# Performance work log

Hardware: AMD Instinct MI355X
Metric: run time of the kernel (lower is better)

The kernel has to match this reference:

```python
import jax, jax.numpy as jnp
import numpy as np

B, T, C, H = 2, 2048, 1024, 16
D = C // H  # head dim = 64

def setup_inputs() -> dict:
    key = jax.random.key(0)
    k1, k2 = jax.random.split(key)
    x = jax.random.normal(k1, (B, T, C), dtype=jnp.float32)
    W_attn = jax.random.normal(k2, (3 * C, C), dtype=jnp.float32) * 0.02
    return {"x": x, "W_attn": W_attn}

def reference(x, W_attn):
    Bx, Tx, Cx = x.shape
    qkv = jnp.einsum('btc,fc->btf', x, W_attn)  # fused QKV projection (bias=False)
    q, k, v = jnp.split(qkv, 3, axis=-1)
    # [B, H, T, D]
    q = q.reshape(Bx, Tx, H, D).transpose(0, 2, 1, 3)
    k = k.reshape(Bx, Tx, H, D).transpose(0, 2, 1, 3)
    v = v.reshape(Bx, Tx, H, D).transpose(0, 2, 1, 3)
    scale = 1.0 / jnp.sqrt(jnp.asarray(D, dtype=q.dtype))
    scores = jnp.einsum('bhqd,bhkd->bhqk', q, k) * scale  # [B,H,T,T]
    causal = jnp.tril(jnp.ones((Tx, Tx), dtype=bool))
    scores = jnp.where(causal[None, None], scores, jnp.asarray(-jnp.inf, dtype=scores.dtype))
    attn = jax.nn.softmax(scores, axis=-1)
    y = jnp.einsum('bhqk,bhkd->bhqd', attn, v)
    y = y.transpose(0, 2, 1, 3).reshape(Bx, Tx, Cx)  # merge heads; dropout=0 at eval
    return y
```

## Files before the change

### kernel.cpp

```cpp
#include <hip/hip_runtime.h>
#include <hip/hip_bf16.h>

#define Bn 2
#define Tn 2048
#define Cn 1024
#define Hn 16
#define Dn 64
#define Mdim 4096
#define Ndim 3072
#define Kdim 1024

typedef unsigned short u16;
typedef __attribute__((ext_vector_type(8))) short bf16x8;
typedef __attribute__((ext_vector_type(4))) float f32x4;

__device__ __forceinline__ u16 f2bf(float v) {
    unsigned int x = __builtin_bit_cast(unsigned int, v);
    unsigned int r = (x + 0x7fffu + ((x >> 16) & 1u)) >> 16;
    return (u16)r;
}

__device__ __forceinline__ unsigned int cvt_pk_bf16(float lo, float hi) {
    unsigned int r;
    asm("v_cvt_pk_bf16_f32 %0, %1, %2" : "=v"(r) : "v"(lo), "v"(hi));
    return r;
}

__device__ __forceinline__ void async16(const void* g, void* l) {
    __builtin_amdgcn_global_load_lds(
        (const __attribute__((address_space(1))) void*)g,
        (__attribute__((address_space(3))) void*)(unsigned int)(unsigned long long)l,
        16, 0, 0);
}

__device__ __forceinline__ int probe_inline(const unsigned int* __restrict__ X, int tid) {
    const int lane = tid & 63;
    int cnt = 0;
    #pragma unroll
    for (int i = 0; i < 8; i++) {
        unsigned int e = (X[lane * 8 + i] >> 7) & 0xFFu;
        cnt += (e >= 100u && e < 134u) ? 1 : 0;
    }
    #pragma unroll
    for (int off = 1; off < 64; off <<= 1) cnt += __shfl_xor(cnt, off);
    return cnt > 256 ? 1 : 0;
}

#define NXC ((size_t)Mdim * Kdim / 8)
#define NWC ((size_t)Ndim * Kdim / 8)

__global__ __launch_bounds__(256) void convert_in(
        const void* __restrict__ Xv, const void* __restrict__ Wv,
        u16* __restrict__ Xb, u16* __restrict__ Wb, int* __restrict__ flag) {
    const int isbf = probe_inline((const unsigned int*)Xv, threadIdx.x);
    if (blockIdx.x == 0 && threadIdx.x == 0) *flag = isbf;
    size_t i = (size_t)blockIdx.x * 256 + threadIdx.x;
    if (i >= NXC + NWC) return;
    const void* src; u16* dst; size_t off;
    if (i < NXC) { src = Xv; dst = Xb; off = i; }
    else         { src = Wv; dst = Wb; off = i - NXC; }
    if (isbf) {
        ((uint4*)dst)[off] = ((const uint4*)src)[off];
    } else {
        const float4* s = (const float4*)src + off * 2;
        float4 a = s[0], b = s[1];
        ((uint4*)dst)[off] = (uint4){cvt_pk_bf16(a.x, a.y), cvt_pk_bf16(a.z, a.w),
                                     cvt_pk_bf16(b.x, b.y), cvt_pk_bf16(b.z, b.w)};
    }
}

#define NTq (Kdim / 64)
#define QSCL 0.1803368867f

#define PBAR() do { asm volatile("" ::: "memory"); \
                    __builtin_amdgcn_s_barrier();  \
                    asm volatile("" ::: "memory"); } while (0)
#define VMW(n) asm volatile("s_waitcnt vmcnt(" #n ")" ::: "memory")

#define STGA(QIDX, BUF, KOFF) \
    async16(Xb + (size_t)(m0 + (QIDX) * 64 + srow) * Kdim + (KOFF) + gc, \
            &sA[BUF][(QIDX) * 4096 + w * 512])
#define STGB(QIDX, BUF, KOFF) \
    async16(Wb + (size_t)(n0 + (QIDX) * 64 + srow) * Kdim + (KOFF) + gc, \
            &sB[BUF][(QIDX) * 4096 + w * 512])

#define RDAh(FR, MQ, BUF) do {                                             \
    _Pragma("unroll")                                                      \
    for (int mt = 0; mt < 4; mt++) {                                       \
        const u16* p = &sA[BUF][(wm + (MQ) * 64 + mt * 16 + r16) * 64];    \
        FR[mt][0] = *(const bf16x8*)(p + cx0);                             \
        FR[mt][1] = *(const bf16x8*)(p + (cx0 ^ 32));                      \
    } } while (0)

#define RDBall(BUF) do {                                                   \
    _Pragma("unroll")                                                      \
    for (int nt = 0; nt < 3; nt++) {                                       \
        const u16* p = &sB[BUF][(wn + nt * 16 + r16) * 64];                \
        bfr[nt][0] = *(const bf16x8*)(p + cx0);                            \
        bfr[nt][1] = *(const bf16x8*)(p + (cx0 ^ 32));                     \
    } } while (0)

#define MMH(BASE, FR) do {                                                 \
    _Pragma("unroll")                                                      \
    for (int mt = 0; mt < 4; mt++)                                         \
        _Pragma("unroll")                                                  \
        for (int nt = 0; nt < 3; nt++) {                                   \
            acc[(BASE)+mt][nt] = __builtin_amdgcn_mfma_f32_16x16x32_bf16(  \
                FR[mt][0], bfr[nt][0], acc[(BASE)+mt][nt], 0, 0, 0);       \
            acc[(BASE)+mt][nt] = __builtin_amdgcn_mfma_f32_16x16x32_bf16(  \
                FR[mt][1], bfr[nt][1], acc[(BASE)+mt][nt], 0, 0, 0);       \
        }                                                                  \
} while (0)

__global__ __launch_bounds__(512, 2) void qkv_gemm(
        const u16* __restrict__ Xb, const u16* __restrict__ Wb,
        u16* __restrict__ Q, u16* __restrict__ Kc, u16* __restrict__ Vt) {
    __shared__ __align__(16) u16 sA[2][256 * 64];
    __shared__ __align__(16) u16 sB[2][192 * 64];

    const int tid  = threadIdx.x;
    const int lane = tid & 63;
    const int w    = tid >> 6;
    const int quad = lane >> 4;
    const int r16  = lane & 15;
    const int wm   = (w >> 2) * 128;
    const int wn   = (w & 3) * 48;

    const int l0 = blockIdx.x;
    const int nl = (l0 & 7) * 32 + (l0 >> 3);
    const int m0 = (nl >> 4) * 256;
    const int n0 = (nl & 15) * 192;

    const int lr   = lane >> 3;
    const int gc   = ((lane & 7) ^ lr) * 8;
    const int srow = w * 8 + lr;

    const int cx0 = (quad ^ (r16 & 7)) * 8;

    f32x4 acc[8][3];
    #pragma unroll
    for (int i = 0; i < 8; i++)
        #pragma unroll
        for (int j = 0; j < 3; j++)
            acc[i][j] = (f32x4){0.f, 0.f, 0.f, 0.f};

    bf16x8 af[4][2], ag[4][2];
    bf16x8 bfr[3][2];

    #pragma unroll
    for (int q = 0; q < 4; q++) STGA(q, 0, 0);
    #pragma unroll
    for (int q = 0; q < 3; q++) STGB(q, 0, 0);
    STGA(0, 1, 64); STGA(2, 1, 64); STGB(0, 1, 64); STGB(1, 1, 64);
    VMW(4);
    PBAR();

    int koff = 0;
    for (int kt = 0; kt < NTq; kt++) {
        const int cur = kt & 1, nxt = cur ^ 1;
        const int kn = koff + 64, kn2 = koff + 128;
        if (kt + 1 < NTq) { STGA(1, nxt, kn); STGA(3, nxt, kn); STGB(2, nxt, kn); }
        RDAh(af, 0, cur);
        RDBall(cur);
        PBAR();
        __builtin_amdgcn_s_setprio(1);
        MMH(0, af);
        __builtin_amdgcn_s_setprio(0);
        PBAR();
        RDAh(ag, 1, cur);
        if (kt + 2 < NTq) { STGA(0, cur, kn2); STGA(2, cur, kn2);
                            STGB(0, cur, kn2); STGB(1, cur, kn2); }
        if (kt + 2 < NTq)      { VMW(4); }
        else if (kt + 1 < NTq) { VMW(0); }
        PBAR();
        __builtin_amdgcn_s_setprio(1);
        MMH(4, ag);
        __builtin_amdgcn_s_setprio(0);
        PBAR();
        koff = kn;
    }

    #pragma unroll
    for (int mh = 0; mh < 2; mh++)
    #pragma unroll
    for (int mt = 0; mt < 4; mt++)
    #pragma unroll
    for (int nt = 0; nt < 3; nt++) {
        f32x4 v4 = acc[mh * 4 + mt][nt];
        const int mBase = m0 + wm + mh * 64 + mt * 16 + quad * 4;
        const int f = n0 + wn + nt * 16 + r16;
        const int sect = f >> 10;
        const int b = mBase >> 11;
        const int t0 = mBase & 2047;
        const int h = (f >> 6) & 15;
        const int d = f & 63;
        const int bh = b * Hn + h;
        if (sect == 0) {
            unsigned int u01 = cvt_pk_bf16(v4[0] * QSCL, v4[1] * QSCL);
            unsigned int u23 = cvt_pk_bf16(v4[2] * QSCL, v4[3] * QSCL);
            u16* qp = Q + ((size_t)(bh * Tn + t0)) * Dn + d;
            qp[0]      = (u16)u01;
            qp[Dn]     = (u16)(u01 >> 16);
            qp[2 * Dn] = (u16)u23;
            qp[3 * Dn] = (u16)(u23 >> 16);
        } else if (sect == 1) {
            unsigned int u01 = cvt_pk_bf16(v4[0], v4[1]);
            unsigned int u23 = cvt_pk_bf16(v4[2], v4[3]);
            u16* kp = Kc + ((size_t)(bh * Tn + t0)) * Dn + d;
            kp[0]      = (u16)u01;
            kp[Dn]     = (u16)(u01 >> 16);
            kp[2 * Dn] = (u16)u23;
            kp[3 * Dn] = (u16)(u23 >> 16);
        } else {
            uint2 pk2 = {cvt_pk_bf16(v4[0], v4[1]), cvt_pk_bf16(v4[2], v4[3])};
            *(uint2*)(Vt + ((size_t)(bh * Dn + d)) * Tn + t0) = pk2;
        }
    }
}


#define SWZ(R, C) ((R) * 64 + (((C) * 8) ^ (((R) & 7) << 3)))

#define ASTG(KB, BUF) do {                                                     \
    const int kbase_ = (KB) * 64;                                              \
    if (w < 2) {                                                               \
        _Pragma("unroll")                                                      \
        for (int i_ = 0; i_ < 4; i_++) {                                       \
            const int seg = w * 4 + i_;            \
            async16(Kc + qkBase + (size_t)(kbase_ + seg * 8 + rl) * Dn + gc8,  \
                    &sK[BUF][seg * 512]);                                      \
        }                                                                      \
    } else {                                                                   \
        _Pragma("unroll")                                                      \
        for (int i_ = 0; i_ < 4; i_++) {                                       \
            const int seg = (w - 2) * 4 + i_;    \
            async16(Vt + vBase + (size_t)(seg * 8 + rl) * Tn + kbase_ + gc8,   \
                    &sV[BUF][seg * 512]);                                      \
        }                                                                      \
    }                                                                          \
} while (0)

#define ACOMP(KB, BUF) do {                                                    \
    const int kbase_ = (KB) * 64;                                              \
    const bool diag_ = ((KB) == nkb - 1);                                      \
    bf16x8 kf[4][2], vf[4][2];                                                 \
    _Pragma("unroll")                                                          \
    for (int nt = 0; nt < 4; nt++) {                                           \
        kf[nt][0] = *(const bf16x8*)&sK[BUF][SWZ(nt * 16 + r16, quad)];        \
        kf[nt][1] = *(const bf16x8*)&sK[BUF][SWZ(nt * 16 + r16, 4 + quad)];    \
    }                                                                          \
    _Pragma("unroll")                                                          \
    for (int dt = 0; dt < 4; dt++) {                                           \
        vf[dt][0] = *(const bf16x8*)&sV[BUF][SWZ(dt * 16 + r16, quad)];        \
        vf[dt][1] = *(const bf16x8*)&sV[BUF][SWZ(dt * 16 + r16, 4 + quad)];    \
    }                                                                          \
    _Pragma("unroll")                                                          \
    for (int mt = 0; mt < 2; mt++) {                                           \
        f32x4 s[4];                                                            \
        __builtin_amdgcn_s_setprio(1);                                         \
        _Pragma("unroll")                                                      \
        for (int nt = 0; nt < 4; nt++) {                                       \
            f32x4 z = (f32x4){-11.5415603f, -11.5415603f, -11.5415603f, -11.5415603f}; \
            z = __builtin_amdgcn_mfma_f32_16x16x32_bf16(kf[nt][0], aq[mt][0], z, 0, 0, 0); \
            z = __builtin_amdgcn_mfma_f32_16x16x32_bf16(kf[nt][1], aq[mt][1], z, 0, 0, 0); \
            s[nt] = z;                                                         \
        }                                                                      \
        __builtin_amdgcn_s_setprio(0);                                         \
        if (diag_) {                                                           \
            const int query = qw0 + mt * 16 + r16;                             \
            _Pragma("unroll")                                                  \
            for (int nt = 0; nt < 4; nt++)                                     \
                _Pragma("unroll")                                              \
                for (int r = 0; r < 4; r++) {                                  \
                    int key = kbase_ + nt * 16 + quad * 4 + r;                 \
                    if (key > query) s[nt][r] = -1e30f;                        \
                }                                                              \
        }                                                                      \
        unsigned int pk[4][2];                                                 \
        _Pragma("unroll")                                                      \
        for (int nt = 0; nt < 4; nt++) {                                       \
            float p0 = __builtin_amdgcn_exp2f(s[nt][0]);                       \
            float p1 = __builtin_amdgcn_exp2f(s[nt][1]);                       \
            float p2 = __builtin_amdgcn_exp2f(s[nt][2]);                       \
            float p3 = __builtin_amdgcn_exp2f(s[nt][3]);                       \
            lacc[mt] += (p0 + p1) + (p2 + p3);                                 \
            pk[nt][0] = cvt_pk_bf16(p0, p1);                                   \
            pk[nt][1] = cvt_pk_bf16(p2, p3);                                   \
        }                                                                      \
        _Pragma("unroll")                                                      \
        for (int kc = 0; kc < 2; kc++) {                                       \
            int4 bq;                                                           \
            _Pragma("unroll")                                                  \
            for (int h_ = 0; h_ < 2; h_++) {                                   \
                unsigned int a = pk[kc * 2 + 0][h_];                           \
                unsigned int b = pk[kc * 2 + 1][h_];                           \
                auto t = __builtin_amdgcn_permlane32_swap(a, b, false, false); \
                auto u = __builtin_amdgcn_permlane16_swap(t[0], t[1], false, false); \
                ((unsigned int*)&bq)[0 + h_] = u[0];                           \
                ((unsigned int*)&bq)[2 + h_] = u[1];                           \
            }                                                                  \
            bf16x8 bqv = __builtin_bit_cast(bf16x8, bq);                       \
            __builtin_amdgcn_s_setprio(1);                                     \
            _Pragma("unroll")                                                  \
            for (int dt = 0; dt < 4; dt++)                                     \
                o[mt][dt] = __builtin_amdgcn_mfma_f32_16x16x32_bf16(           \
                    vf[dt][kc], bqv, o[mt][dt], 0, 0, 0);                      \
            __builtin_amdgcn_s_setprio(0);                                     \
        }                                                                      \
    }                                                                          \
} while (0)

__global__ __launch_bounds__(256, 2) void attn(
        const u16* __restrict__ Q, const u16* __restrict__ Kc,
        const u16* __restrict__ Vt, void* __restrict__ Y,
        const int* __restrict__ flag) {
    __shared__ __align__(16) u16 sK[4][4096];
    __shared__ __align__(16) u16 sV[4][4096];

    const int isbf = *flag;
    const int tid  = threadIdx.x;
    const int lane = tid & 63;
    const int w    = tid >> 6;
    const int quad = lane >> 4;
    const int r16  = lane & 15;
    const int bid  = blockIdx.x;
    const int bh   = bid & (Bn * Hn - 1);
    const int half = bid >> 8;
    const int j    = (bid & 255) >> 5;
    const int qt   = half ? j : (15 - j);
    const int qw0  = qt * 128 + w * 32;
    const int nt   = 2 * qt + 2;
    const int nkb  = 2 * qt + 1 + (w >> 1);
    const size_t qkBase = (size_t)bh * Tn * Dn;
    const size_t vBase  = (size_t)bh * Dn * Tn;
    const int bb = bh >> 4, hh = bh & 15;

    const int rl  = lane >> 3;
    const int gc8 = (((lane & 7) ^ rl)) * 8;

    bf16x8 aq[2][2];
    #pragma unroll
    for (int mt = 0; mt < 2; mt++) {
        const u16* qp = Q + qkBase + (size_t)(qw0 + mt * 16 + r16) * Dn;
        aq[mt][0] = *(const bf16x8*)(qp + quad * 8);
        aq[mt][1] = *(const bf16x8*)(qp + 32 + quad * 8);
    }

    float lacc[2] = {0.f, 0.f};
    f32x4 o[2][4];
    #pragma unroll
    for (int mt = 0; mt < 2; mt++)
        #pragma unroll
        for (int dt = 0; dt < 4; dt++) o[mt][dt] = (f32x4){0.f, 0.f, 0.f, 0.f};

    ASTG(0, 0);
    ASTG(1, 1);
    VMW(4);
    PBAR();

    for (int i = 0; i < nt; i++) {
        if (i + 2 < nt)      { ASTG(i + 2, (i + 2) & 3); VMW(8); }
        else if (i + 1 < nt) { VMW(4); }
        else                 { VMW(0); }
        PBAR();
        if (i < nkb) ACOMP(i, i & 3);
    }

    #pragma unroll
    for (int mt = 0; mt < 2; mt++) {
        float den = lacc[mt];
        den += __shfl_xor(den, 16);
        den += __shfl_xor(den, 32);
        float rden = 1.f / fmaxf(den, 1e-30f);
        int t = qw0 + mt * 16 + r16;
        #pragma unroll
        for (int dt = 0; dt < 4; dt++) {
            float v0 = o[mt][dt][0] * rden;
            float v1 = o[mt][dt][1] * rden;
            float v2 = o[mt][dt][2] * rden;
            float v3 = o[mt][dt][3] * rden;
            int c = hh * Dn + dt * 16 + quad * 4;
            size_t idx = ((size_t)(bb * Tn + t)) * Cn + c;
            if (isbf) {
                uint2 pk2 = {cvt_pk_bf16(v0, v1), cvt_pk_bf16(v2, v3)};
                *(uint2*)((u16*)Y + idx) = pk2;
            } else {
                float4 f4 = {v0, v1, v2, v3};
                *(float4*)((float*)Y + idx) = f4;
            }
        }
    }
}

extern "C" void kernel_launch(void* const* d_in, const int* in_sizes, int n_in,
                              void* d_out, int out_size, void* d_ws, size_t ws_size,
                              hipStream_t stream) {
    const void* X = d_in[0];
    const void* W = d_in[1];
    void* Y = d_out;

    const size_t per = (size_t)Bn * Hn * Tn * Dn;
    int* flag = (int*)d_ws;
    u16* Q  = (u16*)((char*)d_ws + 256);
    u16* Kc = Q + per;
    u16* Vt = Kc + per;
    u16* Xb = Vt + per;
    u16* Wb = Xb + (size_t)Mdim * Kdim;

    {
        const size_t nch = NXC + NWC;
        convert_in<<<dim3((unsigned)((nch + 255) / 256)), 256, 0, stream>>>(X, W, Xb, Wb, flag);
    }
    qkv_gemm<<<dim3((Mdim / 256) * (Ndim / 192)), 512, 0, stream>>>(Xb, Wb, Q, Kc, Vt);
    attn<<<dim3(Bn * Hn * (Tn / 128)), 256, 0, stream>>>(Q, Kc, Vt, Y, flag);
}
```

Measured before the change: 140.1 us.

## Restructure QKV GEMM main loop into finer phases with full-tile prefetch two ahead

Result: no change. 137.7 us (median of 2 runs) (-1.7%).

```diff
diff --git a/kernel.cpp b/kernel.cpp
--- a/kernel.cpp
+++ b/kernel.cpp
@@ -92,24 +92,44 @@
         FR[mt][1] = *(const bf16x8*)(p + (cx0 ^ 32));                      \
     } } while (0)
 
-#define RDBall(BUF) do {                                                   \
+#define RDB01(BUF) do {                                                    \
     _Pragma("unroll")                                                      \
-    for (int nt = 0; nt < 3; nt++) {                                       \
+    for (int nt = 0; nt < 2; nt++) {                                       \
         const u16* p = &sB[BUF][(wn + nt * 16 + r16) * 64];                \
         bfr[nt][0] = *(const bf16x8*)(p + cx0);                            \
         bfr[nt][1] = *(const bf16x8*)(p + (cx0 ^ 32));                     \
     } } while (0)
 
-#define MMH(BASE, FR) do {                                                 \
+#define RDB2(BUF) do {                                                     \
+    const u16* p = &sB[BUF][(wn + 2 * 16 + r16) * 64];                     \
+    bfr[2][0] = *(const bf16x8*)(p + cx0);                                 \
+    bfr[2][1] = *(const bf16x8*)(p + (cx0 ^ 32));                          \
+} while (0)
+
+#define MM01(BASE, FR) do {                                                \
+    __builtin_amdgcn_s_setprio(1);                                         \
     _Pragma("unroll")                                                      \
     for (int mt = 0; mt < 4; mt++)                                         \
         _Pragma("unroll")                                                  \
-        for (int nt = 0; nt < 3; nt++) {                                   \
+        for (int nt = 0; nt < 2; nt++) {                                   \
             acc[(BASE)+mt][nt] = __builtin_amdgcn_mfma_f32_16x16x32_bf16(  \
                 FR[mt][0], bfr[nt][0], acc[(BASE)+mt][nt], 0, 0, 0);       \
             acc[(BASE)+mt][nt] = __builtin_amdgcn_mfma_f32_16x16x32_bf16(  \
                 FR[mt][1], bfr[nt][1], acc[(BASE)+mt][nt], 0, 0, 0);       \
         }                                                                  \
+    __builtin_amdgcn_s_setprio(0);                                         \
+} while (0)
+
+#define MM2(BASE, FR) do {                                                 \
+    __builtin_amdgcn_s_setprio(1);                                         \
+    _Pragma("unroll")                                                      \
+    for (int mt = 0; mt < 4; mt++) {                                       \
+        acc[(BASE)+mt][2] = __builtin_amdgcn_mfma_f32_16x16x32_bf16(       \
+            FR[mt][0], bfr[2][0], acc[(BASE)+mt][2], 0, 0, 0);             \
+        acc[(BASE)+mt][2] = __builtin_amdgcn_mfma_f32_16x16x32_bf16(       \
+            FR[mt][1], bfr[2][1], acc[(BASE)+mt][2], 0, 0, 0);             \
+    }                                                                      \
+    __builtin_amdgcn_s_setprio(0);                                         \
 } while (0)
 
 __global__ __launch_bounds__(512, 2) void qkv_gemm(
@@ -151,33 +171,39 @@
     for (int q = 0; q < 4; q++) STGA(q, 0, 0);
     #pragma unroll
     for (int q = 0; q < 3; q++) STGB(q, 0, 0);
-    STGA(0, 1, 64); STGA(2, 1, 64); STGB(0, 1, 64); STGB(1, 1, 64);
-    VMW(4);
+    #pragma unroll
+    for (int q = 0; q < 4; q++) STGA(q, 1, 64);
+    #pragma unroll
+    for (int q = 0; q < 3; q++) STGB(q, 1, 64);
+    VMW(7);
     PBAR();
 
     int koff = 0;
     for (int kt = 0; kt < NTq; kt++) {
-        const int cur = kt & 1, nxt = cur ^ 1;
-        const int kn = koff + 64, kn2 = koff + 128;
-        if (kt + 1 < NTq) { STGA(1, nxt, kn); STGA(3, nxt, kn); STGB(2, nxt, kn); }
+        const int cur = kt & 1;
+        const int kn2 = koff + 128;
+        const bool pf = (kt + 2 < NTq);
         RDAh(af, 0, cur);
-        RDBall(cur);
-        PBAR();
-        __builtin_amdgcn_s_setprio(1);
-        MMH(0, af);
-        __builtin_amdgcn_s_setprio(0);
+        RDB01(cur);
+        PBAR();
+        MM01(0, af);
+        PBAR();
+        RDB2(cur);
+        if (pf) { STGA(0, cur, kn2); STGA(2, cur, kn2); }
+        PBAR();
+        MM2(0, af);
         PBAR();
         RDAh(ag, 1, cur);
-        if (kt + 2 < NTq) { STGA(0, cur, kn2); STGA(2, cur, kn2);
-                            STGB(0, cur, kn2); STGB(1, cur, kn2); }
-        if (kt + 2 < NTq)      { VMW(4); }
+        if (pf) { STGB(0, cur, kn2); STGB(1, cur, kn2); STGB(2, cur, kn2); }
+        PBAR();
+        MM01(4, ag);
+        PBAR();
+        if (pf) { STGA(1, cur, kn2); STGA(3, cur, kn2); VMW(7); }
         else if (kt + 1 < NTq) { VMW(0); }
         PBAR();
-        __builtin_amdgcn_s_setprio(1);
-        MMH(4, ag);
-        __builtin_amdgcn_s_setprio(0);
-        PBAR();
-        koff = kn;
+        MM2(4, ag);
+        PBAR();
+        koff += 64;
     }
 
     #pragma unroll
```
